# Performance work log

Measured on AMD Instinct MI355X. Metric: run time of the kernel, lower is better.

Reference implementation:

```python
import jax, jax.numpy as jnp
import numpy as np

B, C, N, K = 8, 256, 4096, 16

def setup_inputs() -> dict:
    key = jax.random.key(0)
    k1, k2, k3 = jax.random.split(key, 3)
    x = jax.random.normal(k1, (B, C, N, 1), dtype=jnp.float32)
    edge_index = jax.random.randint(k2, (2, B, N, K), 0, N, dtype=jnp.int64)
    eps = jnp.zeros((1,), dtype=jnp.float32)
    W = jax.random.normal(k3, (C, C), dtype=jnp.float32) * (1.0 / np.sqrt(C))
    b = jnp.zeros((C,), dtype=jnp.float32)
    return {"x": x, "edge_index": edge_index, "eps": eps, "W": W, "b": b}

def reference(x, edge_index, eps, W, b):
    # x: [B, C, N, 1]; edge_index: [2, B, N, K]
    idx = edge_index[0]                                  # [B, N, K] neighbor ids
    x_sq = x[..., 0]                                     # [B, C, N]
    # batched_index_select: gather neighbor features -> [B, C, N, K]
    gath = jnp.take_along_axis(
        x_sq, idx.reshape(B, 1, N * K).astype(jnp.int32), axis=2
    ).reshape(B, C, N, K)
    x_j = jnp.sum(gath, axis=-1, keepdims=True)          # [B, C, N, 1]
    h = (1.0 + eps[0]) * x + x_j                         # GIN update
    # BasicConv: 1x1 Conv2d + bias + ReLU
    out = jnp.einsum('oc,bcnk->bonk', W, h) + b[None, :, None, None]
    return jax.nn.relu(out)
```

## Files before the change

kernel.cpp:

```cpp
#include <hip/hip_runtime.h>
#include <stdint.h>

#define BB 8
#define CC 256
#define NN 4096
#define KK 16
#define NT 32

typedef float f32x4 __attribute__((ext_vector_type(4)));
typedef short bf16x8 __attribute__((ext_vector_type(8)));

__device__ __forceinline__ ushort f2bf(float f) {
  union { float f; uint32_t u; } v; v.f = f;
  uint32_t r = v.u + 0x7FFFu + ((v.u >> 16) & 1u);
  return (ushort)(r >> 16);
}
__device__ __forceinline__ float bf2f(ushort h) {
  union { uint32_t u; float f; } v; v.u = ((uint32_t)h) << 16;
  return v.f;
}

__global__ __launch_bounds__(256) void k_transpose(
    const float* __restrict__ x, ushort* __restrict__ xT)
{
  __shared__ float tile[64][68];
  const int b  = blockIdx.z;
  const int c0 = blockIdx.y * 64;
  const int n0 = blockIdx.x * 64;
  const int t  = threadIdx.x;
  {
    const int r  = t >> 2;
    const int cs = (t & 3) * 16;
    const float* xp = x + ((size_t)b * CC + c0 + r) * NN + n0 + cs;
    #pragma unroll
    for (int i = 0; i < 4; ++i) {
      float4 v = *(const float4*)(xp + i * 4);
      *(float4*)&tile[r][cs + i * 4] = v;
    }
  }
  __syncthreads();
  const int nl = t >> 2;
  const int cl = (t & 3) * 16;
  union { ushort s[16]; uint4 q[2]; } pk;
  #pragma unroll
  for (int i = 0; i < 16; ++i) pk.s[i] = f2bf(tile[cl + i][nl]);
  uint4* dst = (uint4*)(xT + ((size_t)b * NN + n0 + nl) * CC + c0 + cl);
  dst[0] = pk.q[0];
  dst[1] = pk.q[1];
}

__global__ __launch_bounds__(256) void k_wconv(
    const float* __restrict__ W, ushort* __restrict__ Wfrag)
{
  const int t  = threadIdx.x;
  const int o  = blockIdx.x * 4 + (t >> 6);
  const int k0 = (t & 63) * 4;
  float4 v = *(const float4*)(W + (size_t)o * CC + k0);
  ushort4 h;
  h.x = f2bf(v.x); h.y = f2bf(v.y); h.z = f2bf(v.z); h.w = f2bf(v.w);
  const int kc = k0 >> 5, ks = k0 & 31;
  *(ushort4*)(Wfrag + ((size_t)(kc * CC + o)) * 32 + ks) = h;
}

__global__ __launch_bounds__(256) void k_fused(
    const ushort* __restrict__ xT, const int* __restrict__ edge0,
    const float* __restrict__ eps, const ushort* __restrict__ Wfrag,
    const float* __restrict__ bias, float* __restrict__ out)
{
  __shared__ ushort hLds[NT][264];
  const int bid = blockIdx.x;
  const int b   = bid & 7;
  const int n0  = (bid >> 3) * NT;
  const int t    = threadIdx.x;
  const int wave = t >> 6, lane = t & 63;
  const float epsv = 1.0f + eps[0];
  const ushort* xb = xT + (size_t)b * NN * CC;
  const int c4 = lane * 4;

  for (int i = 0; i < NT / 4; ++i) {
    const int nl = wave * (NT / 4) + i;
    const int n  = n0 + nl;
    ushort4 sv = *(const ushort4*)(xb + (size_t)n * CC + c4);
    float a0 = bf2f(sv.x) * epsv;
    float a1 = bf2f(sv.y) * epsv;
    float a2 = bf2f(sv.z) * epsv;
    float a3 = bf2f(sv.w) * epsv;
    const int4* epv = (const int4*)(edge0 + ((size_t)b * NN + n) * KK);
    int4 e0 = epv[0], e1 = epv[1], e2 = epv[2], e3 = epv[3];
    const int js[16] = {e0.x, e0.y, e0.z, e0.w, e1.x, e1.y, e1.z, e1.w,
                        e2.x, e2.y, e2.z, e2.w, e3.x, e3.y, e3.z, e3.w};
    #pragma unroll
    for (int k = 0; k < KK; ++k) {
      ushort4 g = *(const ushort4*)(xb + (size_t)js[k] * CC + c4);
      a0 += bf2f(g.x); a1 += bf2f(g.y); a2 += bf2f(g.z); a3 += bf2f(g.w);
    }
    ushort4 o4;
    o4.x = f2bf(a0); o4.y = f2bf(a1); o4.z = f2bf(a2); o4.w = f2bf(a3);
    *(ushort4*)&hLds[nl][c4] = o4;
  }
  __syncthreads();

  f32x4 acc[4][NT / 16];
  #pragma unroll
  for (int m = 0; m < 4; ++m)
    #pragma unroll
    for (int nn = 0; nn < NT / 16; ++nn) acc[m][nn] = (f32x4){0.f, 0.f, 0.f, 0.f};

  const int lrow = lane & 15;
  const int kgrp = lane >> 4;
  const int o0   = wave * 64;

  #pragma unroll
  for (int kc = 0; kc < 8; ++kc) {
    const int cs = kgrp * 8;
    bf16x8 afr[4], bfr[NT / 16];
    #pragma unroll
    for (int m = 0; m < 4; ++m)
      afr[m] = *(const bf16x8*)(Wfrag +
          ((size_t)(kc * CC + o0 + m * 16 + lrow)) * 32 + cs);
    #pragma unroll
    for (int nn = 0; nn < NT / 16; ++nn)
      bfr[nn] = *(const bf16x8*)&hLds[nn * 16 + lrow][kc * 32 + cs];
    #pragma unroll
    for (int m = 0; m < 4; ++m)
      #pragma unroll
      for (int nn = 0; nn < NT / 16; ++nn)
        acc[m][nn] = __builtin_amdgcn_mfma_f32_16x16x32_bf16(
            afr[m], bfr[nn], acc[m][nn], 0, 0, 0);
  }

  #pragma unroll
  for (int m = 0; m < 4; ++m) {
    #pragma unroll
    for (int r = 0; r < 4; ++r) {
      const int o  = o0 + m * 16 + kgrp * 4 + r;
      const float bv = bias[o];
      #pragma unroll
      for (int nn = 0; nn < NT / 16; ++nn) {
        const int n = n0 + nn * 16 + lrow;
        float v = acc[m][nn][r] + bv;
        v = v > 0.f ? v : 0.f;
        out[((size_t)b * CC + o) * NN + n] = v;
      }
    }
  }
}

extern "C" void kernel_launch(void* const* d_in, const int* in_sizes, int n_in,
                              void* d_out, int out_size, void* d_ws, size_t ws_size,
                              hipStream_t stream) {
  const float* x    = (const float*)d_in[0];
  const int*   edge = (const int*)d_in[1];
  const float* eps  = (const float*)d_in[2];
  const float* W    = (const float*)d_in[3];
  const float* bias = (const float*)d_in[4];
  float* out = (float*)d_out;

  ushort* xT    = (ushort*)d_ws;
  ushort* Wfrag = xT + (size_t)BB * NN * CC;

  dim3 g0(NN / 64, CC / 64, BB);
  k_transpose<<<g0, 256, 0, stream>>>(x, xT);

  k_wconv<<<CC / 4, 256, 0, stream>>>(W, Wfrag);

  k_fused<<<BB * (NN / NT), 256, 0, stream>>>(xT, edge, eps, Wfrag, bias, out);
}
```

Measured before the change: 128.0 us.

## Merge prep kernels, widen gather loads to 16 bytes, add nontemporal edge/out access

The transpose and weight-conversion kernels are folded into a single launch, with block ids at or above 2048 handling W. The transpose's block-to-tile mapping also changes so consecutive blocks cycle through batches. In the fused kernel, each lane now gathers 8 bf16 channels (16-byte loads) with half a wave per node, unrolled over 4 iterations, to cut load instruction count and raise memory-level parallelism. Edge indices are read with nontemporal loads and the output is written with nontemporal stores to avoid polluting cache, at the risk of different cache behaviour for the gather.

```diff
diff --git a/kernel.cpp b/kernel.cpp
--- a/kernel.cpp
+++ b/kernel.cpp
@@ -9,6 +9,7 @@
 
 typedef float f32x4 __attribute__((ext_vector_type(4)));
 typedef short bf16x8 __attribute__((ext_vector_type(8)));
+typedef int   i32x4 __attribute__((ext_vector_type(4)));
 
 __device__ __forceinline__ ushort f2bf(float f) {
   union { float f; uint32_t u; } v; v.f = f;
@@ -20,14 +21,28 @@
   return v.f;
 }
 
-__global__ __launch_bounds__(256) void k_transpose(
-    const float* __restrict__ x, ushort* __restrict__ xT)
+__global__ __launch_bounds__(256) void k_prep(
+    const float* __restrict__ x, const float* __restrict__ W,
+    ushort* __restrict__ xT, ushort* __restrict__ Wfrag)
 {
+  const int bid = blockIdx.x;
+  const int t   = threadIdx.x;
+  if (bid >= 2048) {
+    const int wb = bid - 2048;
+    const int o  = wb * 4 + (t >> 6);
+    const int k0 = (t & 63) * 4;
+    float4 v = *(const float4*)(W + (size_t)o * CC + k0);
+    ushort4 h;
+    h.x = f2bf(v.x); h.y = f2bf(v.y); h.z = f2bf(v.z); h.w = f2bf(v.w);
+    const int kc = k0 >> 5, ks = k0 & 31;
+    *(ushort4*)(Wfrag + ((size_t)(kc * CC + o)) * 32 + ks) = h;
+    return;
+  }
   __shared__ float tile[64][68];
-  const int b  = blockIdx.z;
-  const int c0 = blockIdx.y * 64;
-  const int n0 = blockIdx.x * 64;
-  const int t  = threadIdx.x;
+  const int b    = bid & 7;
+  const int tl   = bid >> 3;
+  const int c0   = (tl & 3) * 64;
+  const int n0   = (tl >> 2) * 64;
   {
     const int r  = t >> 2;
     const int cs = (t & 3) * 16;
@@ -49,19 +64,6 @@
   dst[1] = pk.q[1];
 }
 
-__global__ __launch_bounds__(256) void k_wconv(
-    const float* __restrict__ W, ushort* __restrict__ Wfrag)
-{
-  const int t  = threadIdx.x;
-  const int o  = blockIdx.x * 4 + (t >> 6);
-  const int k0 = (t & 63) * 4;
-  float4 v = *(const float4*)(W + (size_t)o * CC + k0);
-  ushort4 h;
-  h.x = f2bf(v.x); h.y = f2bf(v.y); h.z = f2bf(v.z); h.w = f2bf(v.w);
-  const int kc = k0 >> 5, ks = k0 & 31;
-  *(ushort4*)(Wfrag + ((size_t)(kc * CC + o)) * 32 + ks) = h;
-}
-
 __global__ __launch_bounds__(256) void k_fused(
     const ushort* __restrict__ xT, const int* __restrict__ edge0,
     const float* __restrict__ eps, const ushort* __restrict__ Wfrag,
@@ -75,28 +77,34 @@
   const int wave = t >> 6, lane = t & 63;
   const float epsv = 1.0f + eps[0];
   const ushort* xb = xT + (size_t)b * NN * CC;
-  const int c4 = lane * 4;
 
-  for (int i = 0; i < NT / 4; ++i) {
-    const int nl = wave * (NT / 4) + i;
+  const int half = lane >> 5;
+  const int cl   = (lane & 31) * 8;
+  #pragma unroll
+  for (int it = 0; it < 4; ++it) {
+    const int nl = wave * 8 + it * 2 + half;
     const int n  = n0 + nl;
-    ushort4 sv = *(const ushort4*)(xb + (size_t)n * CC + c4);
-    float a0 = bf2f(sv.x) * epsv;
-    float a1 = bf2f(sv.y) * epsv;
-    float a2 = bf2f(sv.z) * epsv;
-    float a3 = bf2f(sv.w) * epsv;
-    const int4* epv = (const int4*)(edge0 + ((size_t)b * NN + n) * KK);
-    int4 e0 = epv[0], e1 = epv[1], e2 = epv[2], e3 = epv[3];
+    bf16x8 sv = *(const bf16x8*)(xb + (size_t)n * CC + cl);
+    float a[8];
+    #pragma unroll
+    for (int j = 0; j < 8; ++j) a[j] = bf2f((ushort)sv[j]) * epsv;
+    const i32x4* epv = (const i32x4*)(edge0 + ((size_t)b * NN + n) * KK);
+    i32x4 e0 = __builtin_nontemporal_load(epv + 0);
+    i32x4 e1 = __builtin_nontemporal_load(epv + 1);
+    i32x4 e2 = __builtin_nontemporal_load(epv + 2);
+    i32x4 e3 = __builtin_nontemporal_load(epv + 3);
     const int js[16] = {e0.x, e0.y, e0.z, e0.w, e1.x, e1.y, e1.z, e1.w,
                         e2.x, e2.y, e2.z, e2.w, e3.x, e3.y, e3.z, e3.w};
     #pragma unroll
     for (int k = 0; k < KK; ++k) {
-      ushort4 g = *(const ushort4*)(xb + (size_t)js[k] * CC + c4);
-      a0 += bf2f(g.x); a1 += bf2f(g.y); a2 += bf2f(g.z); a3 += bf2f(g.w);
+      bf16x8 g = *(const bf16x8*)(xb + (size_t)js[k] * CC + cl);
+      #pragma unroll
+      for (int j = 0; j < 8; ++j) a[j] += bf2f((ushort)g[j]);
     }
-    ushort4 o4;
-    o4.x = f2bf(a0); o4.y = f2bf(a1); o4.z = f2bf(a2); o4.w = f2bf(a3);
-    *(ushort4*)&hLds[nl][c4] = o4;
+    union { ushort s[8]; bf16x8 v; } pk;
+    #pragma unroll
+    for (int j = 0; j < 8; ++j) pk.s[j] = f2bf(a[j]);
+    *(bf16x8*)&hLds[nl][cl] = pk.v;
   }
   __syncthreads();
 
@@ -140,7 +148,7 @@
         const int n = n0 + nn * 16 + lrow;
         float v = acc[m][nn][r] + bv;
         v = v > 0.f ? v : 0.f;
-        out[((size_t)b * CC + o) * NN + n] = v;
+        __builtin_nontemporal_store(v, &out[((size_t)b * CC + o) * NN + n]);
       }
     }
   }
@@ -159,10 +167,7 @@
   ushort* xT    = (ushort*)d_ws;
   ushort* Wfrag = xT + (size_t)BB * NN * CC;
 
-  dim3 g0(NN / 64, CC / 64, BB);
-  k_transpose<<<g0, 256, 0, stream>>>(x, xT);
-
-  k_wconv<<<CC / 4, 256, 0, stream>>>(W, Wfrag);
+  k_prep<<<2048 + 64, 256, 0, stream>>>(x, W, xT, Wfrag);
 
   k_fused<<<BB * (NN / NT), 256, 0, stream>>>(xT, edge, eps, Wfrag, bias, out);
 }
```

Measured after the change: 121.1 us. -5.4%, faster.
